# Optimization experiments

Measured on AMD Instinct MI355X. Metric: run time of the kernel, lower is better.

The kernel has to match this reference:

```python
import jax, jax.numpy as jnp
import numpy as np

N_NODES = 32768
N_EDGES = 524288
EPS = 1e-5

def _layernorm(h):
    mu = jnp.mean(h, axis=-1, keepdims=True)
    var = jnp.var(h, axis=-1, keepdims=True)
    return (h - mu) / jnp.sqrt(var + EPS)

def _leaky_relu(h):
    return jnp.where(h >= 0, h, 0.01 * h)

def setup_inputs() -> dict:
    key = jax.random.key(0)
    ks = jax.random.split(key, 16)
    F, H, D = 256, 256, 1024
    x = jax.random.normal(ks[0], (N_NODES, F), dtype=jnp.float32)
    src = jax.random.randint(ks[1], (N_EDGES,), 0, N_NODES, dtype=jnp.int32)
    dst = jax.random.randint(ks[2], (N_EDGES,), 0, N_NODES, dtype=jnp.int32)
    dims = [F, H, H, H, D]
    params = {}
    for i in range(4):
        params[f"W{i+1}"] = jax.random.normal(ks[3 + i], (dims[i], dims[i + 1]), dtype=jnp.float32) * (1.0 / np.sqrt(dims[i]))
        params[f"b{i+1}"] = jnp.zeros((dims[i + 1],), dtype=jnp.float32)
    Wm = jax.random.normal(ks[8], (D, D), dtype=jnp.float32) * (1.0 / np.sqrt(D))
    bm = jnp.zeros((D,), dtype=jnp.float32)
    Ws = jax.random.normal(ks[9], (D, D), dtype=jnp.float32) * (1.0 / np.sqrt(D))
    bs = jnp.zeros((D,), dtype=jnp.float32)
    return dict(x=x, src=src, dst=dst, W1=params["W1"], b1=params["b1"], W2=params["W2"], b2=params["b2"], W3=params["W3"], b3=params["b3"], W4=params["W4"], b4=params["b4"], Wm=Wm, bm=bm, Ws=Ws, bs=bs, batch_b=128, nodes_per=256)

def reference(x, src, dst, W1, b1, W2, b2, W3, b3, W4, b4, Wm, bm, Ws, bs, batch_b, nodes_per):
    # DGL GraphConv norm='both': out = D_in^{-1/2} * A @ (D_out^{-1/2} * h) @ W + b
    ones = jnp.ones((src.shape[0],), dtype=x.dtype)
    out_deg = jax.ops.segment_sum(ones, src, num_segments=N_NODES)
    in_deg = jax.ops.segment_sum(ones, dst, num_segments=N_NODES)
    ns = jnp.where(out_deg > 0, jax.lax.rsqrt(out_deg), 1.0)[:, None]
    nd = jnp.where(in_deg > 0, jax.lax.rsqrt(in_deg), 1.0)[:, None]

    def gconv(h, W, b):
        if W.shape[0] <= W.shape[1]:  # aggregate first, then project (in <= out)
            m = (h * ns)[src]
            agg = jax.ops.segment_sum(m, dst, num_segments=N_NODES) * nd
            return agg @ W + b
        else:  # project first
            h = (h * ns) @ W
            agg = jax.ops.segment_sum(h[src], dst, num_segments=N_NODES) * nd
            return agg + b

    h = x
    for (W, b) in [(W1, b1), (W2, b2), (W3, b3), (W4, b4)]:
        h = _layernorm(_leaky_relu(gconv(h, W, b)))
    h = h.reshape(batch_b, nodes_per, -1)  # [B, N_per, D]
    h = jnp.mean(h, axis=1)                # AvePool over nodes
    h = _layernorm(h)
    mean = h @ Wm + bm
    log_std = h @ Ws + bs
    return (mean, log_std)
```

## Files before the change

### kernel.cpp

```cpp
#include <hip/hip_runtime.h>

#define N_NODES 32768
#define N_EDGES 524288

typedef __attribute__((ext_vector_type(8))) short short8;
typedef __attribute__((ext_vector_type(4))) float floatx4;

#define GLOBAL_AS __attribute__((address_space(1)))
#define LDS_AS __attribute__((address_space(3)))

__device__ __forceinline__ unsigned short f2bf(float x) {
    union { float f; unsigned u; } v; v.f = x;
    unsigned r = v.u + 0x7FFF + ((v.u >> 16) & 1);
    return (unsigned short)(r >> 16);
}
__device__ __forceinline__ float bf2f(unsigned short u) {
    union { unsigned u; float f; } v; v.u = ((unsigned)u) << 16;
    return v.f;
}


__global__ __launch_bounds__(256) void k_hist(const int* __restrict__ src,
                                              const int* __restrict__ dst,
                                              unsigned int* __restrict__ histOut32,
                                              unsigned int* __restrict__ histIn32) {
    __shared__ unsigned int hOut[8192];
    __shared__ unsigned int hIn[8192];
    int t = threadIdx.x, b = blockIdx.x;
    for (int i = t; i < 8192; i += 256) { hOut[i] = 0; hIn[i] = 0; }
    __syncthreads();
    int base = b * 4096;
    for (int i = t; i < 4096; i += 256) {
        int s = src[base + i], d = dst[base + i];
        atomicAdd(&hOut[s >> 2], 1u << ((s & 3) * 8));
        atomicAdd(&hIn[d >> 2], 1u << ((d & 3) * 8));
    }
    __syncthreads();
    for (int i = t; i < 8192; i += 256) {
        histOut32[b * 8192 + i] = hOut[i];
        histIn32[b * 8192 + i] = hIn[i];
    }
}

__global__ __launch_bounds__(256) void k_merge_p1(const unsigned int* __restrict__ histIn32,
                                                  const unsigned int* __restrict__ histOut32,
                                                  unsigned int* __restrict__ partIn,
                                                  unsigned int* __restrict__ partOut) {
    int g = blockIdx.x * 256 + threadIdx.x;
    int bg = blockIdx.y;
    unsigned int si = 0, so = 0;
#pragma unroll
    for (int j = 0; j < 16; j++) {
        si += histIn32[(bg * 16 + j) * 8192 + g];
        so += histOut32[(bg * 16 + j) * 8192 + g];
    }
    partIn[bg * 8192 + g] = si;
    partOut[bg * 8192 + g] = so;
}

__global__ __launch_bounds__(256) void k_merge_p2(const unsigned int* __restrict__ histIn32,
                                                  const unsigned int* __restrict__ partIn,
                                                  const unsigned int* __restrict__ partOut,
                                                  unsigned int* __restrict__ pre32,
                                                  int* __restrict__ in_deg,
                                                  float* __restrict__ ns,
                                                  float* __restrict__ nd) {
    int g = blockIdx.x * 256 + threadIdx.x;
    int bg = blockIdx.y;
    unsigned int run = 0;
    for (int b2 = 0; b2 < bg; b2++) run += partIn[b2 * 8192 + g];
    for (int j = 0; j < 16; j++) {
        int b = bg * 16 + j;
        pre32[b * 8192 + g] = run;
        run += histIn32[b * 8192 + g];
    }
    if (bg == 7) {
        int r0 = run & 255, r1 = (run >> 8) & 255, r2 = (run >> 16) & 255, r3 = (run >> 24) & 255;
        in_deg[g * 4 + 0] = r0; in_deg[g * 4 + 1] = r1;
        in_deg[g * 4 + 2] = r2; in_deg[g * 4 + 3] = r3;
        nd[g * 4 + 0] = r0 > 0 ? rsqrtf((float)r0) : 1.0f;
        nd[g * 4 + 1] = r1 > 0 ? rsqrtf((float)r1) : 1.0f;
        nd[g * 4 + 2] = r2 > 0 ? rsqrtf((float)r2) : 1.0f;
        nd[g * 4 + 3] = r3 > 0 ? rsqrtf((float)r3) : 1.0f;
    }
    if (bg == 0) {
        unsigned int to = 0;
#pragma unroll
        for (int b2 = 0; b2 < 8; b2++) to += partOut[b2 * 8192 + g];
        int r0 = to & 255, r1 = (to >> 8) & 255, r2 = (to >> 16) & 255, r3 = (to >> 24) & 255;
        ns[g * 4 + 0] = r0 > 0 ? rsqrtf((float)r0) : 1.0f;
        ns[g * 4 + 1] = r1 > 0 ? rsqrtf((float)r1) : 1.0f;
        ns[g * 4 + 2] = r2 > 0 ? rsqrtf((float)r2) : 1.0f;
        ns[g * 4 + 3] = r3 > 0 ? rsqrtf((float)r3) : 1.0f;
    }
}

__global__ __launch_bounds__(256) void k_scanA(const int* __restrict__ in_deg,
                                               int* __restrict__ row_ptr,
                                               int* __restrict__ blkSum) {
    __shared__ int part[256];
    int t = threadIdx.x, b = blockIdx.x;
    int base = (b * 256 + t) * 4;
    int l0 = in_deg[base], l1 = in_deg[base + 1], l2 = in_deg[base + 2], l3 = in_deg[base + 3];
    part[t] = l0 + l1 + l2 + l3;
    __syncthreads();
    for (int off = 1; off < 256; off <<= 1) {
        int v = (t >= off) ? part[t - off] : 0;
        __syncthreads();
        part[t] += v;
        __syncthreads();
    }
    int excl = (t == 0) ? 0 : part[t - 1];
    row_ptr[base] = excl;
    row_ptr[base + 1] = excl + l0;
    row_ptr[base + 2] = excl + l0 + l1;
    row_ptr[base + 3] = excl + l0 + l1 + l2;
    if (t == 255) blkSum[b] = part[255];
}

__global__ __launch_bounds__(256) void k_scanC(const int* __restrict__ blkSum,
                                               int* __restrict__ row_ptr) {
    __shared__ int soff;
    int t = threadIdx.x, b = blockIdx.x;
    if (t == 0) {
        int s = 0;
        for (int i = 0; i < b; i++) s += blkSum[i];
        soff = s;
    }
    __syncthreads();
    int base = (b * 256 + t) * 4;
    row_ptr[base] += soff; row_ptr[base + 1] += soff;
    row_ptr[base + 2] += soff; row_ptr[base + 3] += soff;
    if (b == 31 && t == 255) row_ptr[N_NODES] = soff + blkSum[31];
}

__global__ __launch_bounds__(256) void k_place(const int* __restrict__ src,
                                               const int* __restrict__ dst,
                                               const unsigned int* __restrict__ pre32,
                                               const int* __restrict__ row_ptr,
                                               int* __restrict__ csr_src) {
    __shared__ unsigned int cur[8192];
    int t = threadIdx.x, b = blockIdx.x;
    for (int i = t; i < 8192; i += 256) cur[i] = 0;
    __syncthreads();
    int base = b * 4096;
    const unsigned int* preb = pre32 + b * 8192;
    for (int i = t; i < 4096; i += 256) {
        int s = src[base + i], d = dst[base + i];
        int sh = (d & 3) * 8;
        unsigned int old = atomicAdd(&cur[d >> 2], 1u << sh);
        int rank = (old >> sh) & 255;
        int pb = (preb[d >> 2] >> sh) & 255;
        csr_src[row_ptr[d] + pb + rank] = s;
    }
}

struct TransDescs {
    const float* W[6];
    unsigned short* Wt[6];
    int K[6], N[6];
    int end[6];
};

__global__ __launch_bounds__(256) void k_transpose_all(TransDescs d) {
    int id = blockIdx.x, s = 0;
#pragma unroll
    for (int i = 0; i < 6; i++) if (id >= d.end[i]) s = i + 1;
    int base = (s == 0) ? 0 : d.end[s - 1];
    int t = id - base;
    int K = d.K[s], N = d.N[s];
    int ncols = N >> 5;
    int n0 = (t % ncols) * 32, k0 = (t / ncols) * 32;
    const float* W = d.W[s];
    unsigned short* Wt = d.Wt[s];
    __shared__ float tile[32][33];
    int tx = threadIdx.x & 31, ty = threadIdx.x >> 5;
    for (int r = 0; r < 32; r += 8)
        tile[ty + r][tx] = W[(size_t)(k0 + ty + r) * N + n0 + tx];
    __syncthreads();
    for (int r = 0; r < 32; r += 8)
        Wt[(size_t)(n0 + ty + r) * K + k0 + tx] = f2bf(tile[tx][ty + r]);
}

__global__ __launch_bounds__(256) void k_scale_x(const float* __restrict__ x,
                                                 const float* __restrict__ ns,
                                                 unsigned short* __restrict__ xsb) {
    int i = blockIdx.x * 256 + threadIdx.x;
    float4 v = ((const float4*)x)[i];
    int n = i >> 6;
    int f = (i & 63) * 4;
    float sc = ns[n];
    ushort4 o;
    o.x = f2bf(v.x * sc); o.y = f2bf(v.y * sc);
    o.z = f2bf(v.z * sc); o.w = f2bf(v.w * sc);
    size_t off = (size_t)(f >> 6) * (N_NODES * 64) + (size_t)n * 64 + (f & 63);
    *(ushort4*)(xsb + off) = o;
}

__global__ __launch_bounds__(512, 4) void fused_layer(
        const unsigned short* __restrict__ hs,
        const int* __restrict__ row_ptr,
        const int* __restrict__ csr_src,
        const float* __restrict__ nd,
        const unsigned short* __restrict__ Bt,
        const float* __restrict__ bias,
        const float* __restrict__ ns,
        unsigned short* __restrict__ ho) {
    __shared__ __align__(16) unsigned short At[8 * 2048];
    __shared__ __align__(16) unsigned short Bs[2][256 * 32];
    __shared__ int eIdx[2048];
    __shared__ int rp[65];
    __shared__ float sSum[4][64], sSum2[4][64], sMa[64], sMb[64];
    const int tid = threadIdx.x;
    const int lane = tid & 63;
    const int w = tid >> 6;
    const int n0 = blockIdx.x * 64;
    const int K = 256;

    const int pr = lane >> 3;
    const int uu = (lane & 7) ^ pr;
    const int rowInGrp = pr * 2 + (uu >> 2);
    const int kc = (uu & 3) * 8;
    const unsigned short* gB = Bt + (size_t)(w * 32 + rowInGrp) * K + kc;
    const int bBase = (w * 32) * 32;
#define STAGEB(buf_, koff_)                                                              \
    {                                                                                    \
        unsigned short* lB = Bs[buf_] + bBase;                                           \
        __builtin_amdgcn_global_load_lds((const GLOBAL_AS short*)(gB + (koff_)),         \
                                         (LDS_AS short*)lB, 16, 0, 0);                   \
        __builtin_amdgcn_global_load_lds((const GLOBAL_AS short*)(gB + (koff_) + (size_t)16 * K), \
                                         (LDS_AS short*)(lB + 16 * 32), 16, 0, 0);       \
    }
    STAGEB(0, 0)

    if (tid <= 64) rp[tid] = row_ptr[n0 + tid];
    __syncthreads();
    const int ebeg = rp[0];
    const int ecount = rp[64] - ebeg;
    const int ecached = ecount < 2048 ? ecount : 2048;
    for (int i = tid; i < ecached; i += 512) eIdx[i] = csr_src[ebeg + i];
    __syncthreads();

    const int r = tid >> 3;
    const int fs = tid & 7;
    const int beg = rp[r] - ebeg, end = rp[r + 1] - ebeg;
    const float sc = nd[n0 + r];
    const int rowpair = r >> 1;
    unsigned short* atp = At + rowpair * 64 +
                          (((((r & 1) << 2) | (fs & 3)) ^ (rowpair & 7)) << 3);

    auto sweep = [&](auto fetch) {
        for (int c = 0; c < 4; c++) {
            const unsigned short* hp = hs + (size_t)c * (N_NODES * 64) + fs * 8;
            float acc[8];
#pragma unroll
            for (int k = 0; k < 8; k++) acc[k] = 0.f;
            int e = beg;
            for (; e + 8 <= end; e += 8) {
                int s0 = fetch(e),     s1 = fetch(e + 1), s2 = fetch(e + 2), s3 = fetch(e + 3);
                int s4 = fetch(e + 4), s5 = fetch(e + 5), s6 = fetch(e + 6), s7 = fetch(e + 7);
                short8 v0 = *(const short8*)(hp + (size_t)s0 * 64);
                short8 v1 = *(const short8*)(hp + (size_t)s1 * 64);
                short8 v2 = *(const short8*)(hp + (size_t)s2 * 64);
                short8 v3 = *(const short8*)(hp + (size_t)s3 * 64);
                short8 v4 = *(const short8*)(hp + (size_t)s4 * 64);
                short8 v5 = *(const short8*)(hp + (size_t)s5 * 64);
                short8 v6 = *(const short8*)(hp + (size_t)s6 * 64);
                short8 v7 = *(const short8*)(hp + (size_t)s7 * 64);
#pragma unroll
                for (int k = 0; k < 8; k++)
                    acc[k] += ((bf2f((unsigned short)v0[k]) + bf2f((unsigned short)v1[k])) +
                               (bf2f((unsigned short)v2[k]) + bf2f((unsigned short)v3[k]))) +
                              ((bf2f((unsigned short)v4[k]) + bf2f((unsigned short)v5[k])) +
                               (bf2f((unsigned short)v6[k]) + bf2f((unsigned short)v7[k])));
            }
            for (; e + 2 <= end; e += 2) {
                int s0 = fetch(e), s1 = fetch(e + 1);
                short8 v0 = *(const short8*)(hp + (size_t)s0 * 64);
                short8 v1 = *(const short8*)(hp + (size_t)s1 * 64);
#pragma unroll
                for (int k = 0; k < 8; k++)
                    acc[k] += bf2f((unsigned short)v0[k]) + bf2f((unsigned short)v1[k]);
            }
            if (e < end) {
                int s = fetch(e);
                short8 v = *(const short8*)(hp + (size_t)s * 64);
#pragma unroll
                for (int k = 0; k < 8; k++) acc[k] += bf2f((unsigned short)v[k]);
            }
            short8 o;
#pragma unroll
            for (int k = 0; k < 8; k++) o[k] = (short)f2bf(acc[k] * sc);
            *(short8*)(atp + (c * 2 + (fs >> 2)) * 2048) = o;
        }
    };
    if (ecount <= 2048)
        sweep([&](int e) { return eIdx[e]; });
    else
        sweep([&](int e) { return csr_src[ebeg + e]; });

    const int wr = (w >> 2) * 32;
    const int wc = (w & 3) * 64;
    floatx4 acc2[2][4];
#pragma unroll
    for (int i = 0; i < 2; i++)
#pragma unroll
        for (int j = 0; j < 4; j++) acc2[i][j] = (floatx4){0.f, 0.f, 0.f, 0.f};
    const int q = lane >> 4;
    const int ln = lane & 15;
    const int uf = (((ln & 1) << 2) | q) ^ ((ln >> 1) & 7);

    int buf = 0;
    for (int k0 = 0; k0 < K; k0 += 32) {
        __syncthreads();
        if (k0 + 32 < K) STAGEB(buf ^ 1, k0 + 32)
        const unsigned short* rA = At + (k0 >> 5) * 2048;
        const unsigned short* rB = Bs[buf];
        short8 af[2], bfr[4];
#pragma unroll
        for (int i = 0; i < 2; i++)
            af[i] = *(const short8*)(rA + (((wr + i * 16 + ln) >> 1) << 6) + uf * 8);
#pragma unroll
        for (int j = 0; j < 4; j++)
            bfr[j] = *(const short8*)(rB + (((wc + j * 16 + ln) >> 1) << 6) + uf * 8);
#pragma unroll
        for (int i = 0; i < 2; i++)
#pragma unroll
            for (int j = 0; j < 4; j++)
                acc2[i][j] = __builtin_amdgcn_mfma_f32_16x16x32_bf16(af[i], bfr[j], acc2[i][j], 0, 0, 0);
        buf ^= 1;
    }
#undef STAGEB

    float bcol[4];
#pragma unroll
    for (int j = 0; j < 4; j++) bcol[j] = bias[wc + j * 16 + ln];
    const int wcIdx = w & 3;
#pragma unroll
    for (int i = 0; i < 2; i++) {
#pragma unroll
        for (int rr = 0; rr < 4; rr++) {
            float s = 0.f, s2 = 0.f;
#pragma unroll
            for (int j = 0; j < 4; j++) {
                float v = acc2[i][j][rr] + bcol[j];
                v = v >= 0.f ? v : 0.01f * v;
                s += v; s2 += v * v;
            }
#pragma unroll
            for (int off = 8; off > 0; off >>= 1) {
                s += __shfl_down(s, off, 16);
                s2 += __shfl_down(s2, off, 16);
            }
            if (ln == 0) {
                int row = wr + i * 16 + q * 4 + rr;
                sSum[wcIdx][row] = s;
                sSum2[wcIdx][row] = s2;
            }
        }
    }
    __syncthreads();
    if (tid < 64) {
        float su = sSum[0][tid] + sSum[1][tid] + sSum[2][tid] + sSum[3][tid];
        float su2 = sSum2[0][tid] + sSum2[1][tid] + sSum2[2][tid] + sSum2[3][tid];
        float mu = su * (1.0f / 256.0f);
        float var = su2 * (1.0f / 256.0f) - mu * mu;
        float rs = rsqrtf(var + 1e-5f);
        float nsv = ns[n0 + tid];
        sMa[tid] = rs * nsv;
        sMb[tid] = -mu * rs * nsv;
    }
    __syncthreads();
#pragma unroll
    for (int i = 0; i < 2; i++) {
#pragma unroll
        for (int rr = 0; rr < 4; rr++) {
            int row = wr + i * 16 + q * 4 + rr;
            float a = sMa[row], bb = sMb[row];
#pragma unroll
            for (int j = 0; j < 4; j++) {
                float v = acc2[i][j][rr] + bcol[j];
                v = v >= 0.f ? v : 0.01f * v;
                int col = wc + j * 16 + ln;
                size_t off = (size_t)(col >> 6) * (N_NODES * 64) +
                             (size_t)(n0 + row) * 64 + (col & 63);
                ho[off] = f2bf(v * a + bb);
            }
        }
    }
}

__global__ __launch_bounds__(512, 4) void fused_layer4(
        const unsigned short* __restrict__ hs,
        const int* __restrict__ row_ptr,
        const int* __restrict__ csr_src,
        const float* __restrict__ nd,
        const unsigned short* __restrict__ Bt,
        const float* __restrict__ bias,
        unsigned short* __restrict__ h4) {
    __shared__ __align__(16) unsigned short At[8 * 2048];
    __shared__ __align__(16) unsigned short Bs[2][256 * 32];
    __shared__ int eIdx[2048];
    __shared__ int rp[65];
    const int tid = threadIdx.x;
    const int lane = tid & 63;
    const int w = tid >> 6;
    const int n0 = blockIdx.x * 64;
    const int K = 256;

    const int pr = lane >> 3;
    const int uu = (lane & 7) ^ pr;
    const int rowInGrp = pr * 2 + (uu >> 2);
    const int kc = (uu & 3) * 8;
    const int bBase = (w * 32) * 32;
#define STAGEB4(buf_, ct_, koff_)                                                        \
    {                                                                                    \
        const unsigned short* gB = Bt + (size_t)((ct_) * 256 + w * 32 + rowInGrp) * K + kc; \
        unsigned short* lB = Bs[buf_] + bBase;                                           \
        __builtin_amdgcn_global_load_lds((const GLOBAL_AS short*)(gB + (koff_)),         \
                                         (LDS_AS short*)lB, 16, 0, 0);                   \
        __builtin_amdgcn_global_load_lds((const GLOBAL_AS short*)(gB + (koff_) + (size_t)16 * K), \
                                         (LDS_AS short*)(lB + 16 * 32), 16, 0, 0);       \
    }
    STAGEB4(0, 0, 0)

    if (tid <= 64) rp[tid] = row_ptr[n0 + tid];
    __syncthreads();
    const int ebeg = rp[0];
    const int ecount = rp[64] - ebeg;
    const int ecached = ecount < 2048 ? ecount : 2048;
    for (int i = tid; i < ecached; i += 512) eIdx[i] = csr_src[ebeg + i];
    __syncthreads();

    const int r = tid >> 3;
    const int fs = tid & 7;
    const int beg = rp[r] - ebeg, end = rp[r + 1] - ebeg;
    const float sc = nd[n0 + r];
    const int rowpair = r >> 1;
    unsigned short* atp = At + rowpair * 64 +
                          (((((r & 1) << 2) | (fs & 3)) ^ (rowpair & 7)) << 3);

    auto sweep = [&](auto fetch) {
        for (int c = 0; c < 4; c++) {
            const unsigned short* hp = hs + (size_t)c * (N_NODES * 64) + fs * 8;
            float acc[8];
#pragma unroll
            for (int k = 0; k < 8; k++) acc[k] = 0.f;
            int e = beg;
            for (; e + 8 <= end; e += 8) {
                int s0 = fetch(e),     s1 = fetch(e + 1), s2 = fetch(e + 2), s3 = fetch(e + 3);
                int s4 = fetch(e + 4), s5 = fetch(e + 5), s6 = fetch(e + 6), s7 = fetch(e + 7);
                short8 v0 = *(const short8*)(hp + (size_t)s0 * 64);
                short8 v1 = *(const short8*)(hp + (size_t)s1 * 64);
                short8 v2 = *(const short8*)(hp + (size_t)s2 * 64);
                short8 v3 = *(const short8*)(hp + (size_t)s3 * 64);
                short8 v4 = *(const short8*)(hp + (size_t)s4 * 64);
                short8 v5 = *(const short8*)(hp + (size_t)s5 * 64);
                short8 v6 = *(const short8*)(hp + (size_t)s6 * 64);
                short8 v7 = *(const short8*)(hp + (size_t)s7 * 64);
#pragma unroll
                for (int k = 0; k < 8; k++)
                    acc[k] += ((bf2f((unsigned short)v0[k]) + bf2f((unsigned short)v1[k])) +
                               (bf2f((unsigned short)v2[k]) + bf2f((unsigned short)v3[k]))) +
                              ((bf2f((unsigned short)v4[k]) + bf2f((unsigned short)v5[k])) +
                               (bf2f((unsigned short)v6[k]) + bf2f((unsigned short)v7[k])));
            }
            for (; e + 2 <= end; e += 2) {
                int s0 = fetch(e), s1 = fetch(e + 1);
                short8 v0 = *(const short8*)(hp + (size_t)s0 * 64);
                short8 v1 = *(const short8*)(hp + (size_t)s1 * 64);
#pragma unroll
                for (int k = 0; k < 8; k++)
                    acc[k] += bf2f((unsigned short)v0[k]) + bf2f((unsigned short)v1[k]);
            }
            if (e < end) {
                int s = fetch(e);
                short8 v = *(const short8*)(hp + (size_t)s * 64);
#pragma unroll
                for (int k = 0; k < 8; k++) acc[k] += bf2f((unsigned short)v[k]);
            }
            short8 o;
#pragma unroll
            for (int k = 0; k < 8; k++) o[k] = (short)f2bf(acc[k] * sc);
            *(short8*)(atp + (c * 2 + (fs >> 2)) * 2048) = o;
        }
    };
    if (ecount <= 2048)
        sweep([&](int e) { return eIdx[e]; });
    else
        sweep([&](int e) { return csr_src[ebeg + e]; });

    const int wr = (w >> 2) * 32;
    const int wc = (w & 3) * 64;
    const int q = lane >> 4;
    const int ln = lane & 15;
    const int uf = (((ln & 1) << 2) | q) ^ ((ln >> 1) & 7);

    int buf = 0;
    for (int ct = 0; ct < 4; ct++) {
        floatx4 acc2[2][4];
#pragma unroll
        for (int i = 0; i < 2; i++)
#pragma unroll
            for (int j = 0; j < 4; j++) acc2[i][j] = (floatx4){0.f, 0.f, 0.f, 0.f};
        for (int k0 = 0; k0 < K; k0 += 32) {
            __syncthreads();
            if (k0 + 32 < K) {
                STAGEB4(buf ^ 1, ct, k0 + 32)
            } else if (ct < 3) {
                STAGEB4(buf ^ 1, ct + 1, 0)
            }
            const unsigned short* rA = At + (k0 >> 5) * 2048;
            const unsigned short* rB = Bs[buf];
            short8 af[2], bfr[4];
#pragma unroll
            for (int i = 0; i < 2; i++)
                af[i] = *(const short8*)(rA + (((wr + i * 16 + ln) >> 1) << 6) + uf * 8);
#pragma unroll
            for (int j = 0; j < 4; j++)
                bfr[j] = *(const short8*)(rB + (((wc + j * 16 + ln) >> 1) << 6) + uf * 8);
#pragma unroll
            for (int i = 0; i < 2; i++)
#pragma unroll
                for (int j = 0; j < 4; j++)
                    acc2[i][j] = __builtin_amdgcn_mfma_f32_16x16x32_bf16(af[i], bfr[j], acc2[i][j], 0, 0, 0);
            buf ^= 1;
        }
#pragma unroll
        for (int i = 0; i < 2; i++) {
#pragma unroll
            for (int rr = 0; rr < 4; rr++) {
                int row = wr + i * 16 + q * 4 + rr;
#pragma unroll
                for (int j = 0; j < 4; j++) {
                    int col = ct * 256 + wc + j * 16 + ln;
                    float v = acc2[i][j][rr] + bias[col];
                    v = v >= 0.f ? v : 0.01f * v;
                    h4[(size_t)(n0 + row) * 1024 + col] = f2bf(v);
                }
            }
        }
    }
#undef STAGEB4
}

__global__ __launch_bounds__(256) void gemm_heads(
        const unsigned short* __restrict__ A,
        const unsigned short* __restrict__ Bt,
        float* __restrict__ P) {
    __shared__ __align__(16) unsigned short As[2][128 * 32];
    __shared__ __align__(16) unsigned short Bs[2][128 * 32];
    const int tid = threadIdx.x;
    const int lane = tid & 63;
    const int w = tid >> 6;
    const int wr = (w >> 1) * 64;
    const int wc = (w & 1) * 64;
    const int colBase = blockIdx.x * 128;
    const int ks = blockIdx.y;
    const int K = 1024;

    floatx4 acc[4][4];
#pragma unroll
    for (int i = 0; i < 4; i++)
#pragma unroll
        for (int j = 0; j < 4; j++) acc[i][j] = (floatx4){0.f, 0.f, 0.f, 0.f};

    const int pr = lane >> 3;
    const int uu = (lane & 7) ^ pr;
    const int srow = w * 32 + pr * 2 + (uu >> 2);
    const int kc = (uu & 3) * 8;
    const unsigned short* gA = A + (size_t)srow * K + ks * 128 + kc;
    const unsigned short* gB = Bt + (size_t)(colBase + srow) * K + ks * 128 + kc;
    const int wbase = (w * 32) * 32;

    const int q = lane >> 4;
    const int ln = lane & 15;
    const int uf = (((ln & 1) << 2) | q) ^ ((ln >> 1) & 7);

    {
        unsigned short* lA = As[0] + wbase;
        unsigned short* lB = Bs[0] + wbase;
        __builtin_amdgcn_global_load_lds((const GLOBAL_AS short*)(gA),
                                         (LDS_AS short*)lA, 16, 0, 0);
        __builtin_amdgcn_global_load_lds((const GLOBAL_AS short*)(gA + (size_t)16 * K),
                                         (LDS_AS short*)(lA + 16 * 32), 16, 0, 0);
        __builtin_amdgcn_global_load_lds((const GLOBAL_AS short*)(gB),
                                         (LDS_AS short*)lB, 16, 0, 0);
        __builtin_amdgcn_global_load_lds((const GLOBAL_AS short*)(gB + (size_t)16 * K),
                                         (LDS_AS short*)(lB + 16 * 32), 16, 0, 0);
    }

    int buf = 0;
    for (int k0 = 0; k0 < 128; k0 += 32) {
        __syncthreads();
        if (k0 + 32 < 128) {
            unsigned short* lA = As[buf ^ 1] + wbase;
            unsigned short* lB = Bs[buf ^ 1] + wbase;
            __builtin_amdgcn_global_load_lds((const GLOBAL_AS short*)(gA + k0 + 32),
                                             (LDS_AS short*)lA, 16, 0, 0);
            __builtin_amdgcn_global_load_lds((const GLOBAL_AS short*)(gA + k0 + 32 + (size_t)16 * K),
                                             (LDS_AS short*)(lA + 16 * 32), 16, 0, 0);
            __builtin_amdgcn_global_load_lds((const GLOBAL_AS short*)(gB + k0 + 32),
                                             (LDS_AS short*)lB, 16, 0, 0);
            __builtin_amdgcn_global_load_lds((const GLOBAL_AS short*)(gB + k0 + 32 + (size_t)16 * K),
                                             (LDS_AS short*)(lB + 16 * 32), 16, 0, 0);
        }
        const unsigned short* rA = As[buf];
        const unsigned short* rB = Bs[buf];
        short8 af[4], bfr[4];
#pragma unroll
        for (int i = 0; i < 4; i++)
            af[i] = *(const short8*)(rA + (((wr + i * 16 + ln) >> 1) << 6) + uf * 8);
#pragma unroll
        for (int j = 0; j < 4; j++)
            bfr[j] = *(const short8*)(rB + (((wc + j * 16 + ln) >> 1) << 6) + uf * 8);
#pragma unroll
        for (int i = 0; i < 4; i++)
#pragma unroll
            for (int j = 0; j < 4; j++)
                acc[i][j] = __builtin_amdgcn_mfma_f32_16x16x32_bf16(af[i], bfr[j], acc[i][j], 0, 0, 0);
        buf ^= 1;
    }
    float* Pk = P + (size_t)ks * 128 * 2048;
#pragma unroll
    for (int i = 0; i < 4; i++) {
#pragma unroll
        for (int j = 0; j < 4; j++) {
#pragma unroll
            for (int r = 0; r < 4; r++) {
                int row = wr + i * 16 + q * 4 + r;
                int col = colBase + wc + j * 16 + ln;
                Pk[(size_t)row * 2048 + col] = acc[i][j][r];
            }
        }
    }
}

__global__ __launch_bounds__(256) void k_heads_reduce(
        const float* __restrict__ P, const float* __restrict__ bm,
        const float* __restrict__ bsd, float* __restrict__ out) {
    int idx = blockIdx.x * 256 + threadIdx.x;
    int row = idx >> 9;
    int col = (idx & 511) * 4;
    floatx4 s = (floatx4){0.f, 0.f, 0.f, 0.f};
#pragma unroll
    for (int p = 0; p < 8; p++)
        s += *(const floatx4*)(P + (size_t)p * 128 * 2048 + (size_t)row * 2048 + col);
    bool hi = col >= 1024;
    const float* bias = hi ? bsd : bm;
    int bc = hi ? col - 1024 : col;
    s += *(const floatx4*)(bias + bc);
    float* o = hi ? (out + (size_t)128 * 1024 + (size_t)row * 1024 + bc)
                  : (out + (size_t)row * 1024 + col);
    *(floatx4*)o = s;
}

__global__ __launch_bounds__(256) void k_lnpool(const unsigned short* __restrict__ h4,
                                                float* __restrict__ partial) {
    const int g = blockIdx.y, p = blockIdx.x;
    const int w = threadIdx.x >> 6, lane = threadIdx.x & 63;
    float acc[16];
#pragma unroll
    for (int k = 0; k < 16; k++) acc[k] = 0.f;
    for (int i = 0; i < 8; i++) {
        int node = (g * 8 + p) * 32 + w * 8 + i;
        const unsigned short* row = h4 + (size_t)node * 1024 + lane * 16;
        short8 a = *(const short8*)row;
        short8 b = *(const short8*)(row + 8);
        float v[16];
#pragma unroll
        for (int k = 0; k < 8; k++) v[k] = bf2f((unsigned short)a[k]);
#pragma unroll
        for (int k = 0; k < 8; k++) v[8 + k] = bf2f((unsigned short)b[k]);
        float s = 0.f, s2 = 0.f;
#pragma unroll
        for (int k = 0; k < 16; k++) { s += v[k]; s2 += v[k] * v[k]; }
#pragma unroll
        for (int off = 32; off > 0; off >>= 1) {
            s += __shfl_down(s, off);
            s2 += __shfl_down(s2, off);
        }
        s = __shfl(s, 0);
        s2 = __shfl(s2, 0);
        float mu = s * (1.0f / 1024.0f);
        float var = s2 * (1.0f / 1024.0f) - mu * mu;
        float rs = rsqrtf(var + 1e-5f);
#pragma unroll
        for (int k = 0; k < 16; k++) acc[k] += (v[k] - mu) * rs;
    }
    __shared__ float red[4][1024];
    float* my = red[w] + lane * 16;
#pragma unroll
    for (int k = 0; k < 16; k++) my[k] = acc[k];
    __syncthreads();
    int t = threadIdx.x;
    floatx4 o = (floatx4){0.f, 0.f, 0.f, 0.f};
#pragma unroll
    for (int w2 = 0; w2 < 4; w2++) {
        const floatx4 v = *(const floatx4*)(red[w2] + t * 4);
        o += v;
    }
    __builtin_nontemporal_store(o, (floatx4*)(partial + (size_t)(g * 8 + p) * 1024 + t * 4));
}

__global__ __launch_bounds__(256) void k_pool_final(const float* __restrict__ partial,
                                                    unsigned short* __restrict__ pooledb) {
    int g = blockIdx.x, t = threadIdx.x;
    int wave = t >> 6;
    float4 a = make_float4(0.f, 0.f, 0.f, 0.f);
    for (int p = 0; p < 8; p++) {
        float4 v = *(const float4*)(partial + (size_t)(g * 8 + p) * 1024 + t * 4);
        a.x += v.x; a.y += v.y; a.z += v.z; a.w += v.w;
    }
    const float invn = 1.0f / 256.0f;
    a.x *= invn; a.y *= invn; a.z *= invn; a.w *= invn;
    float s = a.x + a.y + a.z + a.w;
    float s2 = a.x * a.x + a.y * a.y + a.z * a.z + a.w * a.w;
#pragma unroll
    for (int off = 32; off > 0; off >>= 1) {
        s += __shfl_down(s, off);
        s2 += __shfl_down(s2, off);
    }
    __shared__ float ss[4], ss2[4];
    if ((t & 63) == 0) { ss[wave] = s; ss2[wave] = s2; }
    __syncthreads();
    if (t == 0) {
        float tt = 0.f, tt2 = 0.f;
        for (int w = 0; w < 4; w++) { tt += ss[w]; tt2 += ss2[w]; }
        float mu = tt / 1024.f;
        float var = tt2 / 1024.f - mu * mu;
        ss[0] = mu;
        ss2[0] = rsqrtf(var + 1e-5f);
    }
    __syncthreads();
    float mu = ss[0], inv = ss2[0];
    ushort4 o;
    o.x = f2bf((a.x - mu) * inv); o.y = f2bf((a.y - mu) * inv);
    o.z = f2bf((a.z - mu) * inv); o.w = f2bf((a.w - mu) * inv);
    *(ushort4*)(pooledb + (size_t)g * 1024 + t * 4) = o;
}

extern "C" void kernel_launch(void* const* d_in, const int* in_sizes, int n_in,
                              void* d_out, int out_size, void* d_ws, size_t ws_size,
                              hipStream_t stream) {
    const float* x  = (const float*)d_in[0];
    const int*   src = (const int*)d_in[1];
    const int*   dst = (const int*)d_in[2];
    const float* W1 = (const float*)d_in[3];  const float* b1 = (const float*)d_in[4];
    const float* W2 = (const float*)d_in[5];  const float* b2 = (const float*)d_in[6];
    const float* W3 = (const float*)d_in[7];  const float* b3 = (const float*)d_in[8];
    const float* W4 = (const float*)d_in[9];  const float* b4 = (const float*)d_in[10];
    const float* Wm = (const float*)d_in[11]; const float* bm = (const float*)d_in[12];
    const float* Wsd = (const float*)d_in[13]; const float* bsd = (const float*)d_in[14];
    float* out = (float*)d_out;

    char* w = (char*)d_ws;
    unsigned short* hsbA = (unsigned short*)w; w += (size_t)N_NODES * 256 * 2;
    unsigned short* hsbB = (unsigned short*)w; w += (size_t)N_NODES * 256 * 2;
    unsigned short* h4b  = (unsigned short*)w; w += (size_t)N_NODES * 1024 * 2;
    float* partial = (float*)w; w += (size_t)128 * 8 * 1024 * 4;
    unsigned short* pooledb = (unsigned short*)w; w += (size_t)128 * 1024 * 2;
    unsigned short* W1t = (unsigned short*)w; w += (size_t)256 * 256 * 2;
    unsigned short* W2t = (unsigned short*)w; w += (size_t)256 * 256 * 2;
    unsigned short* W3t = (unsigned short*)w; w += (size_t)256 * 256 * 2;
    unsigned short* W4t = (unsigned short*)w; w += (size_t)256 * 1024 * 2;
    unsigned short* Wmt = (unsigned short*)w; w += (size_t)1024 * 1024 * 2;
    unsigned short* Wst = (unsigned short*)w; w += (size_t)1024 * 1024 * 2;
    float* ns     = (float*)w; w += (size_t)N_NODES * 4;
    float* nd     = (float*)w; w += (size_t)N_NODES * 4;
    unsigned int* histOut32 = (unsigned int*)w; w += (size_t)128 * 8192 * 4;
    unsigned int* histIn32  = (unsigned int*)w; w += (size_t)128 * 8192 * 4;
    unsigned int* pre32     = (unsigned int*)w; w += (size_t)128 * 8192 * 4;
    unsigned int* partIn    = (unsigned int*)w; w += (size_t)8 * 8192 * 4;
    unsigned int* partOut   = (unsigned int*)w; w += (size_t)8 * 8192 * 4;
    int* blkSum   = (int*)w;   w += (size_t)64 * 4;
    int* in_deg   = (int*)w;   w += (size_t)N_NODES * 4;
    int* row_ptr  = (int*)w;   w += (size_t)(N_NODES + 1) * 4;
    int* csr_src  = (int*)w;   w += (size_t)N_EDGES * 4;
    float* headp = (float*)histOut32;

    TransDescs td;
    td.W[0] = W1; td.W[1] = W2; td.W[2] = W3; td.W[3] = W4; td.W[4] = Wm; td.W[5] = Wsd;
    td.Wt[0] = W1t; td.Wt[1] = W2t; td.Wt[2] = W3t; td.Wt[3] = W4t; td.Wt[4] = Wmt; td.Wt[5] = Wst;
    td.K[0] = 256; td.K[1] = 256; td.K[2] = 256; td.K[3] = 256; td.K[4] = 1024; td.K[5] = 1024;
    td.N[0] = 256; td.N[1] = 256; td.N[2] = 256; td.N[3] = 1024; td.N[4] = 1024; td.N[5] = 1024;
    td.end[0] = 64; td.end[1] = 128; td.end[2] = 192; td.end[3] = 448; td.end[4] = 1472; td.end[5] = 2496;
    k_transpose_all<<<2496, 256, 0, stream>>>(td);

    k_hist<<<128, 256, 0, stream>>>(src, dst, histOut32, histIn32);
    k_merge_p1<<<dim3(32, 8), 256, 0, stream>>>(histIn32, histOut32, partIn, partOut);
    k_merge_p2<<<dim3(32, 8), 256, 0, stream>>>(histIn32, partIn, partOut, pre32, in_deg, ns, nd);
    k_scanA<<<32, 256, 0, stream>>>(in_deg, row_ptr, blkSum);
    k_scanC<<<32, 256, 0, stream>>>(blkSum, row_ptr);
    k_place<<<128, 256, 0, stream>>>(src, dst, pre32, row_ptr, csr_src);

    k_scale_x<<<N_NODES * 256 / 1024, 256, 0, stream>>>(x, ns, hsbA);

    const unsigned short* Wts[3] = {W1t, W2t, W3t};
    const float* bs3[3] = {b1, b2, b3};
    unsigned short* tin = hsbA;
    unsigned short* tout = hsbB;
    for (int l = 0; l < 3; l++) {
        fused_layer<<<N_NODES / 64, 512, 0, stream>>>(tin, row_ptr, csr_src, nd,
                                                      Wts[l], bs3[l], ns, tout);
        unsigned short* tmp = tin; tin = tout; tout = tmp;
    }

    fused_layer4<<<N_NODES / 64, 512, 0, stream>>>(tin, row_ptr, csr_src, nd,
                                                   W4t, b4, h4b);

    k_lnpool<<<dim3(8, 128), 256, 0, stream>>>(h4b, partial);
    k_pool_final<<<128, 256, 0, stream>>>(partial, pooledb);

    gemm_heads<<<dim3(16, 8), 256, 0, stream>>>(pooledb, Wmt, headp);
    k_heads_reduce<<<256, 256, 0, stream>>>(headp, bm, bsd, out);
}
```

Baseline: 336.3 us.

## Halve node tile to 32 rows and split gather channels across thread halves

The fused GCN layer kernels now handle 32 nodes per block instead of 64, doubling the grid. Within a block, the two halves of the 512 threads each gather two of the four 64-feature channel chunks, so every thread does half the gather work. LDS buffers shrink and each wave's MFMA tile becomes 16x64, and launch bounds rise to 6 blocks per CU to raise occupancy and latency hiding for the irregular gathers. The trade-off is that each block re-stages the full weight matrix for half as many rows, doubling weight traffic per node, and each wave does fewer MFMAs per LDS load.

```diff
diff --git a/kernel.cpp b/kernel.cpp
--- a/kernel.cpp
+++ b/kernel.cpp
@@ -197,7 +197,7 @@
     *(ushort4*)(xsb + off) = o;
 }
 
-__global__ __launch_bounds__(512, 4) void fused_layer(
+__global__ __launch_bounds__(512, 6) void fused_layer(
         const unsigned short* __restrict__ hs,
         const int* __restrict__ row_ptr,
         const int* __restrict__ csr_src,
@@ -206,15 +206,15 @@
         const float* __restrict__ bias,
         const float* __restrict__ ns,
         unsigned short* __restrict__ ho) {
-    __shared__ __align__(16) unsigned short At[8 * 2048];
+    __shared__ __align__(16) unsigned short At[8 * 1024];
     __shared__ __align__(16) unsigned short Bs[2][256 * 32];
-    __shared__ int eIdx[2048];
-    __shared__ int rp[65];
-    __shared__ float sSum[4][64], sSum2[4][64], sMa[64], sMb[64];
+    __shared__ int eIdx[768];
+    __shared__ int rp[33];
+    __shared__ float sSum[4][32], sSum2[4][32], sMa[32], sMb[32];
     const int tid = threadIdx.x;
     const int lane = tid & 63;
     const int w = tid >> 6;
-    const int n0 = blockIdx.x * 64;
+    const int n0 = blockIdx.x * 32;
     const int K = 256;
 
     const int pr = lane >> 3;
@@ -233,16 +233,18 @@
     }
     STAGEB(0, 0)
 
-    if (tid <= 64) rp[tid] = row_ptr[n0 + tid];
+    if (tid <= 32) rp[tid] = row_ptr[n0 + tid];
     __syncthreads();
     const int ebeg = rp[0];
-    const int ecount = rp[64] - ebeg;
-    const int ecached = ecount < 2048 ? ecount : 2048;
+    const int ecount = rp[32] - ebeg;
+    const int ecached = ecount < 768 ? ecount : 768;
     for (int i = tid; i < ecached; i += 512) eIdx[i] = csr_src[ebeg + i];
     __syncthreads();
 
-    const int r = tid >> 3;
-    const int fs = tid & 7;
+    const int pair = tid & 255;
+    const int half = tid >> 8;
+    const int r = pair >> 3;
+    const int fs = pair & 7;
     const int beg = rp[r] - ebeg, end = rp[r + 1] - ebeg;
     const float sc = nd[n0 + r];
     const int rowpair = r >> 1;
@@ -250,7 +252,7 @@
                           (((((r & 1) << 2) | (fs & 3)) ^ (rowpair & 7)) << 3);
 
     auto sweep = [&](auto fetch) {
-        for (int c = 0; c < 4; c++) {
+        for (int c = half * 2; c < half * 2 + 2; c++) {
             const unsigned short* hp = hs + (size_t)c * (N_NODES * 64) + fs * 8;
             float acc[8];
 #pragma unroll
@@ -291,21 +293,19 @@
             short8 o;
 #pragma unroll
             for (int k = 0; k < 8; k++) o[k] = (short)f2bf(acc[k] * sc);
-            *(short8*)(atp + (c * 2 + (fs >> 2)) * 2048) = o;
+            *(short8*)(atp + (c * 2 + (fs >> 2)) * 1024) = o;
         }
     };
-    if (ecount <= 2048)
+    if (ecount <= 768)
         sweep([&](int e) { return eIdx[e]; });
     else
         sweep([&](int e) { return csr_src[ebeg + e]; });
 
-    const int wr = (w >> 2) * 32;
+    const int wr = (w >> 2) * 16;
     const int wc = (w & 3) * 64;
-    floatx4 acc2[2][4];
-#pragma unroll
-    for (int i = 0; i < 2; i++)
-#pragma unroll
-        for (int j = 0; j < 4; j++) acc2[i][j] = (floatx4){0.f, 0.f, 0.f, 0.f};
+    floatx4 acc2[4];
+#pragma unroll
+    for (int j = 0; j < 4; j++) acc2[j] = (floatx4){0.f, 0.f, 0.f, 0.f};
     const int q = lane >> 4;
     const int ln = lane & 15;
     const int uf = (((ln & 1) << 2) | q) ^ ((ln >> 1) & 7);
@@ -314,20 +314,16 @@
     for (int k0 = 0; k0 < K; k0 += 32) {
         __syncthreads();
         if (k0 + 32 < K) STAGEB(buf ^ 1, k0 + 32)
-        const unsigned short* rA = At + (k0 >> 5) * 2048;
+        const unsigned short* rA = At + (k0 >> 5) * 1024;
         const unsigned short* rB = Bs[buf];
-        short8 af[2], bfr[4];
-#pragma unroll
-        for (int i = 0; i < 2; i++)
-            af[i] = *(const short8*)(rA + (((wr + i * 16 + ln) >> 1) << 6) + uf * 8);
+        short8 af = *(const short8*)(rA + (((wr + ln) >> 1) << 6) + uf * 8);
+        short8 bfr[4];
 #pragma unroll
         for (int j = 0; j < 4; j++)
             bfr[j] = *(const short8*)(rB + (((wc + j * 16 + ln) >> 1) << 6) + uf * 8);
 #pragma unroll
-        for (int i = 0; i < 2; i++)
-#pragma unroll
-            for (int j = 0; j < 4; j++)
-                acc2[i][j] = __builtin_amdgcn_mfma_f32_16x16x32_bf16(af[i], bfr[j], acc2[i][j], 0, 0, 0);
+        for (int j = 0; j < 4; j++)
+            acc2[j] = __builtin_amdgcn_mfma_f32_16x16x32_bf16(af, bfr[j], acc2[j], 0, 0, 0);
         buf ^= 1;
     }
 #undef STAGEB
@@ -337,30 +333,27 @@
     for (int j = 0; j < 4; j++) bcol[j] = bias[wc + j * 16 + ln];
     const int wcIdx = w & 3;
 #pragma unroll
-    for (int i = 0; i < 2; i++) {
-#pragma unroll
-        for (int rr = 0; rr < 4; rr++) {
-            float s = 0.f, s2 = 0.f;
-#pragma unroll
-            for (int j = 0; j < 4; j++) {
-                float v = acc2[i][j][rr] + bcol[j];
-                v = v >= 0.f ? v : 0.01f * v;
-                s += v; s2 += v * v;
-            }
-#pragma unroll
-            for (int off = 8; off > 0; off >>= 1) {
-                s += __shfl_down(s, off, 16);
-                s2 += __shfl_down(s2, off, 16);
-            }
-            if (ln == 0) {
-                int row = wr + i * 16 + q * 4 + rr;
-                sSum[wcIdx][row] = s;
-                sSum2[wcIdx][row] = s2;
-            }
-        }
-    }
-    __syncthreads();
-    if (tid < 64) {
+    for (int rr = 0; rr < 4; rr++) {
+        float s = 0.f, s2 = 0.f;
+#pragma unroll
+        for (int j = 0; j < 4; j++) {
+            float v = acc2[j][rr] + bcol[j];
+            v = v >= 0.f ? v : 0.01f * v;
+            s += v; s2 += v * v;
+        }
+#pragma unroll
+        for (int off = 8; off > 0; off >>= 1) {
+            s += __shfl_down(s, off, 16);
+            s2 += __shfl_down(s2, off, 16);
+        }
+        if (ln == 0) {
+            int row = wr + q * 4 + rr;
+            sSum[wcIdx][row] = s;
+            sSum2[wcIdx][row] = s2;
+        }
+    }
+    __syncthreads();
+    if (tid < 32) {
         float su = sSum[0][tid] + sSum[1][tid] + sSum[2][tid] + sSum[3][tid];
         float su2 = sSum2[0][tid] + sSum2[1][tid] + sSum2[2][tid] + sSum2[3][tid];
         float mu = su * (1.0f / 256.0f);
@@ -372,25 +365,22 @@
     }
     __syncthreads();
 #pragma unroll
-    for (int i = 0; i < 2; i++) {
-#pragma unroll
-        for (int rr = 0; rr < 4; rr++) {
-            int row = wr + i * 16 + q * 4 + rr;
-            float a = sMa[row], bb = sMb[row];
-#pragma unroll
-            for (int j = 0; j < 4; j++) {
-                float v = acc2[i][j][rr] + bcol[j];
-                v = v >= 0.f ? v : 0.01f * v;
-                int col = wc + j * 16 + ln;
-                size_t off = (size_t)(col >> 6) * (N_NODES * 64) +
-                             (size_t)(n0 + row) * 64 + (col & 63);
-                ho[off] = f2bf(v * a + bb);
-            }
-        }
-    }
-}
-
-__global__ __launch_bounds__(512, 4) void fused_layer4(
+    for (int rr = 0; rr < 4; rr++) {
+        int row = wr + q * 4 + rr;
+        float a = sMa[row], bb = sMb[row];
+#pragma unroll
+        for (int j = 0; j < 4; j++) {
+            float v = acc2[j][rr] + bcol[j];
+            v = v >= 0.f ? v : 0.01f * v;
+            int col = wc + j * 16 + ln;
+            size_t off = (size_t)(col >> 6) * (N_NODES * 64) +
+                         (size_t)(n0 + row) * 64 + (col & 63);
+            ho[off] = f2bf(v * a + bb);
+        }
+    }
+}
+
+__global__ __launch_bounds__(512, 6) void fused_layer4(
         const unsigned short* __restrict__ hs,
         const int* __restrict__ row_ptr,
         const int* __restrict__ csr_src,
@@ -398,14 +388,14 @@
         const unsigned short* __restrict__ Bt,
         const float* __restrict__ bias,
         unsigned short* __restrict__ h4) {
-    __shared__ __align__(16) unsigned short At[8 * 2048];
+    __shared__ __align__(16) unsigned short At[8 * 1024];
     __shared__ __align__(16) unsigned short Bs[2][256 * 32];
-    __shared__ int eIdx[2048];
-    __shared__ int rp[65];
+    __shared__ int eIdx[768];
+    __shared__ int rp[33];
     const int tid = threadIdx.x;
     const int lane = tid & 63;
     const int w = tid >> 6;
-    const int n0 = blockIdx.x * 64;
+    const int n0 = blockIdx.x * 32;
     const int K = 256;
 
     const int pr = lane >> 3;
@@ -424,16 +414,18 @@
     }
     STAGEB4(0, 0, 0)
 
-    if (tid <= 64) rp[tid] = row_ptr[n0 + tid];
+    if (tid <= 32) rp[tid] = row_ptr[n0 + tid];
     __syncthreads();
     const int ebeg = rp[0];
-    const int ecount = rp[64] - ebeg;
-    const int ecached = ecount < 2048 ? ecount : 2048;
+    const int ecount = rp[32] - ebeg;
+    const int ecached = ecount < 768 ? ecount : 768;
     for (int i = tid; i < ecached; i += 512) eIdx[i] = csr_src[ebeg + i];
     __syncthreads();
 
-    const int r = tid >> 3;
-    const int fs = tid & 7;
+    const int pair = tid & 255;
+    const int half = tid >> 8;
+    const int r = pair >> 3;
+    const int fs = pair & 7;
     const int beg = rp[r] - ebeg, end = rp[r + 1] - ebeg;
     const float sc = nd[n0 + r];
     const int rowpair = r >> 1;
@@ -441,7 +433,7 @@
                           (((((r & 1) << 2) | (fs & 3)) ^ (rowpair & 7)) << 3);
 
     auto sweep = [&](auto fetch) {
-        for (int c = 0; c < 4; c++) {
+        for (int c = half * 2; c < half * 2 + 2; c++) {
             const unsigned short* hp = hs + (size_t)c * (N_NODES * 64) + fs * 8;
             float acc[8];
 #pragma unroll
@@ -482,15 +474,15 @@
             short8 o;
 #pragma unroll
             for (int k = 0; k < 8; k++) o[k] = (short)f2bf(acc[k] * sc);
-            *(short8*)(atp + (c * 2 + (fs >> 2)) * 2048) = o;
+            *(short8*)(atp + (c * 2 + (fs >> 2)) * 1024) = o;
         }
     };
-    if (ecount <= 2048)
+    if (ecount <= 768)
         sweep([&](int e) { return eIdx[e]; });
     else
         sweep([&](int e) { return csr_src[ebeg + e]; });
 
-    const int wr = (w >> 2) * 32;
+    const int wr = (w >> 2) * 16;
     const int wc = (w & 3) * 64;
     const int q = lane >> 4;
     const int ln = lane & 15;
@@ -498,11 +490,9 @@
 
     int buf = 0;
     for (int ct = 0; ct < 4; ct++) {
-        floatx4 acc2[2][4];
-#pragma unroll
-        for (int i = 0; i < 2; i++)
-#pragma unroll
-            for (int j = 0; j < 4; j++) acc2[i][j] = (floatx4){0.f, 0.f, 0.f, 0.f};
+        floatx4 acc2[4];
+#pragma unroll
+        for (int j = 0; j < 4; j++) acc2[j] = (floatx4){0.f, 0.f, 0.f, 0.f};
         for (int k0 = 0; k0 < K; k0 += 32) {
             __syncthreads();
             if (k0 + 32 < K) {
@@ -510,34 +500,27 @@
             } else if (ct < 3) {
                 STAGEB4(buf ^ 1, ct + 1, 0)
             }
-            const unsigned short* rA = At + (k0 >> 5) * 2048;
+            const unsigned short* rA = At + (k0 >> 5) * 1024;
             const unsigned short* rB = Bs[buf];
-            short8 af[2], bfr[4];
-#pragma unroll
-            for (int i = 0; i < 2; i++)
-                af[i] = *(const short8*)(rA + (((wr + i * 16 + ln) >> 1) << 6) + uf * 8);
+            short8 af = *(const short8*)(rA + (((wr + ln) >> 1) << 6) + uf * 8);
+            short8 bfr[4];
 #pragma unroll
             for (int j = 0; j < 4; j++)
                 bfr[j] = *(const short8*)(rB + (((wc + j * 16 + ln) >> 1) << 6) + uf * 8);
 #pragma unroll
-            for (int i = 0; i < 2; i++)
-#pragma unroll
-                for (int j = 0; j < 4; j++)
-                    acc2[i][j] = __builtin_amdgcn_mfma_f32_16x16x32_bf16(af[i], bfr[j], acc2[i][j], 0, 0, 0);
+            for (int j = 0; j < 4; j++)
+                acc2[j] = __builtin_amdgcn_mfma_f32_16x16x32_bf16(af, bfr[j], acc2[j], 0, 0, 0);
             buf ^= 1;
         }
 #pragma unroll
-        for (int i = 0; i < 2; i++) {
-#pragma unroll
-            for (int rr = 0; rr < 4; rr++) {
-                int row = wr + i * 16 + q * 4 + rr;
-#pragma unroll
-                for (int j = 0; j < 4; j++) {
-                    int col = ct * 256 + wc + j * 16 + ln;
-                    float v = acc2[i][j][rr] + bias[col];
-                    v = v >= 0.f ? v : 0.01f * v;
-                    h4[(size_t)(n0 + row) * 1024 + col] = f2bf(v);
-                }
+        for (int rr = 0; rr < 4; rr++) {
+            int row = wr + q * 4 + rr;
+#pragma unroll
+            for (int j = 0; j < 4; j++) {
+                int col = ct * 256 + wc + j * 16 + ln;
+                float v = acc2[j][rr] + bias[col];
+                v = v >= 0.f ? v : 0.01f * v;
+                h4[(size_t)(n0 + row) * 1024 + col] = f2bf(v);
             }
         }
     }
@@ -801,12 +784,12 @@
     unsigned short* tin = hsbA;
     unsigned short* tout = hsbB;
     for (int l = 0; l < 3; l++) {
-        fused_layer<<<N_NODES / 64, 512, 0, stream>>>(tin, row_ptr, csr_src, nd,
+        fused_layer<<<N_NODES / 32, 512, 0, stream>>>(tin, row_ptr, csr_src, nd,
                                                       Wts[l], bs3[l], ns, tout);
         unsigned short* tmp = tin; tin = tout; tout = tmp;
     }
 
-    fused_layer4<<<N_NODES / 64, 512, 0, stream>>>(tin, row_ptr, csr_src, nd,
+    fused_layer4<<<N_NODES / 32, 512, 0, stream>>>(tin, row_ptr, csr_src, nd,
                                                    W4t, b4, h4b);
 
     k_lnpool<<<dim3(8, 128), 256, 0, stream>>>(h4b, partial);
```

After: 382.7 us. +13.8%, slower.
